# Performance work log

Hardware: AMD Instinct MI355X
Metric: run time of the kernel (lower is better)

The kernel has to match this reference:

```python
import jax, jax.numpy as jnp
import numpy as np

B = 16384      # games
BS = 19        # board size
N2 = BS * BS   # 361
G = 8          # groups per board
S = 4          # stones per group
R = B * G      # total groups
K = R * S      # total stones
M = N2         # hash history length (H*W*history_factor)
I32MIN = np.iinfo(np.int32).min
I32MAX = np.iinfo(np.int32).max
NEG = jnp.float32(-1e9)


def setup_inputs() -> dict:
    key = jax.random.key(0)
    ks = jax.random.split(key, 10)
    logits = jax.random.normal(ks[0], (B, BS, BS), dtype=jnp.float32)
    legal_mask = jax.random.uniform(ks[1], (B, BS, BS)) < 0.7
    current_player = jax.random.randint(ks[2], (B,), 0, 2, dtype=jnp.int32)
    current_hash = jax.random.randint(ks[3], (B,), 0, I32MAX, dtype=jnp.int32)
    hash_history = jax.random.randint(ks[4], (B, M), 0, I32MAX, dtype=jnp.int32)
    move_count = jax.random.randint(ks[5], (B,), 0, M, dtype=jnp.int32)
    ZposT = jax.random.randint(ks[6], (3, N2), 0, I32MAX, dtype=jnp.int32)
    stone_global_index = jax.random.randint(ks[7], (K,), 0, N2, dtype=jnp.int32)
    stone_global_pointer = jnp.arange(R + 1, dtype=jnp.int32) * S          # CSR: stones per group
    group_global_pointer_per_board = jnp.arange(B + 1, dtype=jnp.int32) * G  # CSR: groups per board
    cap_idx = jax.random.randint(ks[8], (B, N2, 4), 0, G, dtype=jnp.int32)
    cap_on = jax.random.uniform(ks[9], (B, N2, 4)) < 0.05
    captured_group_local_index = jnp.where(cap_on, cap_idx, jnp.int32(-1))
    return {
        "logits": logits,
        "legal_mask": legal_mask,
        "current_player": current_player,
        "current_hash": current_hash,
        "hash_history": hash_history,
        "move_count": move_count,
        "ZposT": ZposT,
        "stone_global_index": stone_global_index,
        "stone_global_pointer": stone_global_pointer,
        "group_global_pointer_per_board": group_global_pointer_per_board,
        "captured_group_local_index": captured_group_local_index,
    }


def reference(logits, legal_mask, current_player, current_hash, hash_history,
              move_count, ZposT, stone_global_index, stone_global_pointer,
              group_global_pointer_per_board, captured_group_local_index):
    Bn, H, W = legal_mask.shape
    Rn = stone_global_pointer.shape[0] - 1
    Kn = stone_global_index.shape[0]
    z_empty, z_black, z_white = ZposT[0], ZposT[1], ZposT[2]

    # Placement delta: empty -> current player's stone, for every candidate point. (B, N2)
    placement_delta = z_empty[None, :] ^ jnp.where(
        (current_player == 0)[:, None], z_black[None, :], z_white[None, :])

    # Map each group -> board, each stone -> group (CSR expansion).
    groups_per_board = group_global_pointer_per_board[1:] - group_global_pointer_per_board[:-1]
    group_board = jnp.repeat(jnp.arange(Bn, dtype=jnp.int32), groups_per_board,
                             total_repeat_length=Rn)
    stones_per_group = stone_global_pointer[1:] - stone_global_pointer[:-1]
    group_for_stone = jnp.repeat(jnp.arange(Rn, dtype=jnp.int32), stones_per_group,
                                 total_repeat_length=Kn)
    stone_board = group_board[group_for_stone]

    # Per-stone removal delta: opponent stone -> empty.
    opp_for_stone = (1 - current_player)[stone_board]           # (K,)
    si = stone_global_index.astype(jnp.int32)
    z_opp = ZposT[1 + opp_for_stone, si]
    per_stone_delta = z_opp ^ z_empty[si]                        # (K,) int32

    # Segmented XOR reduction over each group's stones via XOR prefix scan.
    prefix = jax.lax.associative_scan(jnp.bitwise_xor, per_stone_delta)
    start = stone_global_pointer[:-1]
    end = stone_global_pointer[1:]
    end_val = prefix[jnp.clip(end - 1, 0)]
    start_val = jnp.where(start > 0, prefix[jnp.clip(start - 1, 0)], jnp.int32(0))
    group_xor = end_val ^ start_val                              # (R,) per-group removal delta

    # Gather capture deltas for up to 4 captured neighbor groups per candidate move.
    offs = group_global_pointer_per_board[:-1][:, None, None]    # (B,1,1)
    flat_ids = jnp.clip(captured_group_local_index, 0) + offs    # (B,N2,4)
    cap_vals = jnp.where(captured_group_local_index >= 0, group_xor[flat_ids], jnp.int32(0))
    capture_delta = cap_vals[..., 0] ^ cap_vals[..., 1] ^ cap_vals[..., 2] ^ cap_vals[..., 3]

    candidate = current_hash[:, None] ^ placement_delta ^ capture_delta  # (B, N2)

    # Super-ko repeat detection against hash history (mask, sort, searchsorted).
    Mh = hash_history.shape[1]
    valid = jnp.arange(Mh, dtype=jnp.int32)[None, :] < jnp.minimum(move_count, Mh)[:, None]
    masked_hist = jnp.where(valid, hash_history, jnp.int32(I32MIN))
    sorted_hist = jnp.sort(masked_hist, axis=1)
    idx = jnp.clip(
        jax.vmap(lambda h, c: jnp.searchsorted(h, c, side='right'))(sorted_hist, candidate) - 1,
        0)
    found = jnp.take_along_axis(sorted_hist, idx, axis=1)
    repeat = (found == candidate).reshape(Bn, H, W)

    final_mask = legal_mask & ~repeat
    return jnp.where(final_mask, logits, NEG)
```

## Files before the change

kernel.cpp:

```cpp
#include <hip/hip_runtime.h>
#include <stdint.h>

#define N2 361
#define TBL 1024u
#define TBL_MASK 1023u
#define EMPTY 0x80000000u
#define NEGV -998244352.0f

__global__ __launch_bounds__(256) void k_groups(
    const int* __restrict__ current_player,
    const int* __restrict__ ZposT,
    const int* __restrict__ stone_global_index,
    const int* __restrict__ stone_global_pointer,
    unsigned*  __restrict__ gx_out,
    const void* __restrict__ legal_raw,
    unsigned*  __restrict__ fmt_out,
    int packed_bits, int Rn)
{
    const int r = blockIdx.x * 256 + threadIdx.x;

    if (blockIdx.x == 0 && threadIdx.x < 64) {
        const int lane = threadIdx.x;
        const unsigned* lwd = (const unsigned*)legal_raw;
        const unsigned dv0 = lwd[lane];
        const unsigned dv1 = (lane < 27) ? lwd[64 + lane] : 0u;
        auto classify = [](unsigned v) -> unsigned {
            unsigned f = 0;
            #pragma unroll
            for (int j = 0; j < 4; ++j) {
                const unsigned bv = (v >> (8 * j)) & 0xFFu;
                if (bv > 1u) f |= 1u;
                if (j != 0 && bv != 0u) f |= 2u;
            }
            const unsigned x = v & 0xFFFFu, y = v >> 16;
            if ((x && x != 0x3F80u) || (y && y != 0x3F80u)) f |= 4u;
            if (x == 0x3F80u) f |= 8u;
            return f;
        };
        unsigned fcl = classify(dv0);
        if (lane < 27) fcl |= classify(dv1);
        unsigned fa = 0;
        fa |= __ballot(fcl & 1u) ? 1u : 0u;
        fa |= __ballot(fcl & 2u) ? 2u : 0u;
        fa |= __ballot(fcl & 4u) ? 4u : 0u;
        fa |= __ballot(fcl & 8u) ? 8u : 0u;
        unsigned fmt;
        if (packed_bits) fmt = 4u;
        else if (!(fa & 1u)) fmt = (fa & 2u) ? 1u : 0u;
        else if (!(fa & 4u)) fmt = (fa & 8u) ? 2u : 0u;
        else fmt = 1u;
        if (lane == 0) fmt_out[0] = fmt;
    }

    if (r < Rn) {
        const int sp0 = stone_global_pointer[r];
        const int sp1 = stone_global_pointer[r + 1];
        const int b   = r >> 3;
        const int cp  = current_player[b];
        const int opprow = (2 - cp) * N2;
        unsigned x = 0u;
        for (int k = sp0; k < sp1; ++k) {
            const int si = stone_global_index[k];
            x ^= (unsigned)ZposT[opprow + si] ^ (unsigned)ZposT[si];
        }
        gx_out[r] = x;
    }
}

__device__ __forceinline__ unsigned sel8(uint4 a, uint4 b, unsigned i) {
    const unsigned r01 = (i & 1u) ? a.y : a.x;
    const unsigned r23 = (i & 1u) ? a.w : a.z;
    const unsigned r45 = (i & 1u) ? b.y : b.x;
    const unsigned r67 = (i & 1u) ? b.w : b.z;
    const unsigned r03 = (i & 2u) ? r23 : r01;
    const unsigned r47 = (i & 2u) ? r67 : r45;
    return (i & 4u) ? r47 : r03;
}

__global__ __launch_bounds__(384) void k_board(
    const float* __restrict__ logits,
    const void*  __restrict__ legal_raw,
    const int*   __restrict__ current_hash,
    const int*   __restrict__ current_player,
    const int*   __restrict__ hash_history,
    const int*   __restrict__ move_count,
    const int*   __restrict__ ZposT,
    const int4*  __restrict__ captured4,
    const unsigned* __restrict__ gx_ws,
    const unsigned* __restrict__ fmt_ws,
    float* __restrict__ out)
{
    __shared__ unsigned s_tbl[TBL];

    const int b = blockIdx.x;
    const int t = threadIdx.x;
    const size_t bbase = (size_t)b * N2;
    const bool act = t < N2;
    const int tc = act ? t : (N2 - 1);
    const size_t q = bbase + tc;

    int cnt = move_count[b];
    cnt = cnt < 0 ? 0 : (cnt > N2 ? N2 : cnt);
    const int      fmt  = (int)fmt_ws[0];
    const unsigned ch   = (unsigned)current_hash[b];
    const int      cp   = current_player[b];
    const uint4    ga   = *(const uint4*)(gx_ws + b * 8);
    const uint4    gb   = *(const uint4*)(gx_ws + b * 8 + 4);
    const int      prow = (1 + cp) * N2;

    const int   hv  = hash_history[q];
    const int4  cap = captured4[q];
    const float lgt = logits[q];
    unsigned    leg;
    if (fmt == 0)      leg = ((const unsigned*)legal_raw)[q];
    else if (fmt == 1) leg = ((const uint8_t*)legal_raw)[q];
    else if (fmt == 2) leg = ((const uint16_t*)legal_raw)[q];
    else               leg = (((const uint8_t*)legal_raw)[q >> 3] >> (q & 7)) & 1u;
    const unsigned zz = (unsigned)ZposT[tc] ^ (unsigned)ZposT[prow + tc];

    s_tbl[t] = EMPTY;
    s_tbl[t + 384] = EMPTY;
    if (t < (int)TBL - 768) s_tbl[t + 768] = EMPTY;
    __syncthreads();

    if (t < cnt) {
        const unsigned v = (unsigned)hv;
        unsigned slot = v & TBL_MASK;
        while (true) {
            const unsigned old = atomicCAS(&s_tbl[slot], EMPTY, v);
            if (old == EMPTY || old == v) break;
            slot = (slot + 1) & TBL_MASK;
        }
    }

    unsigned capd = 0u;
    if (cap.x >= 0) capd ^= sel8(ga, gb, (unsigned)cap.x & 7u);
    if (cap.y >= 0) capd ^= sel8(ga, gb, (unsigned)cap.y & 7u);
    if (cap.z >= 0) capd ^= sel8(ga, gb, (unsigned)cap.z & 7u);
    if (cap.w >= 0) capd ^= sel8(ga, gb, (unsigned)cap.w & 7u);
    const unsigned cand = ch ^ zz ^ capd;

    __syncthreads();

    bool rep = false;
    {
        unsigned slot = cand & TBL_MASK;
        while (true) {
            const unsigned v = s_tbl[slot];
            if (v == cand) { rep = true; break; }
            if (v == EMPTY) break;
            slot = (slot + 1) & TBL_MASK;
        }
    }

    if (act) {
        const float v = (leg && !rep) ? lgt : NEGV;
        __builtin_nontemporal_store(v, &out[q]);
    }
}

extern "C" void kernel_launch(void* const* d_in, const int* in_sizes, int n_in,
                              void* d_out, int out_size, void* d_ws, size_t ws_size,
                              hipStream_t stream) {
    const float* logits  = (const float*)d_in[0];
    const void*  legal   = (const void*)d_in[1];
    const int*   cur_pl  = (const int*)d_in[2];
    const int*   cur_h   = (const int*)d_in[3];
    const int*   hist    = (const int*)d_in[4];
    const int*   mcount  = (const int*)d_in[5];
    const int*   zpos    = (const int*)d_in[6];
    const int*   sgi     = (const int*)d_in[7];
    const int*   sgp     = (const int*)d_in[8];
    const int4*  cap4    = (const int4*)d_in[10];
    float*       out     = (float*)d_out;

    const int B  = in_sizes[2];
    const int Rn = in_sizes[8] - 1;
    const int packed = (in_sizes[1] != in_sizes[0]);

    unsigned* gx_ws  = (unsigned*)d_ws;
    unsigned* fmt_ws = (unsigned*)((char*)d_ws + (size_t)Rn * 4);

    k_groups<<<(Rn + 255) / 256, 256, 0, stream>>>(
        cur_pl, zpos, sgi, sgp, gx_ws, legal, fmt_ws, packed, Rn);

    k_board<<<B, 384, 0, stream>>>(
        logits, legal, cur_h, cur_pl, hist, mcount, zpos,
        cap4, gx_ws, fmt_ws, out);
}
```

Measured before the change: 218.3 us.

## Make board kernel persistent with double-buffered hash table and register prefetch

```diff
diff --git a/kernel.cpp b/kernel.cpp
--- a/kernel.cpp
+++ b/kernel.cpp
@@ -6,6 +6,7 @@
 #define TBL_MASK 1023u
 #define EMPTY 0x80000000u
 #define NEGV -998244352.0f
+#define NBLK 1280
 
 __global__ __launch_bounds__(256) void k_groups(
     const int* __restrict__ current_player,
@@ -77,6 +78,13 @@
     return (i & 4u) ? r47 : r03;
 }
 
+__device__ __forceinline__ unsigned load_leg(int fmt, const void* p, size_t q) {
+    if (fmt == 0)      return ((const unsigned*)p)[q];
+    else if (fmt == 1) return ((const uint8_t*)p)[q];
+    else if (fmt == 2) return ((const uint16_t*)p)[q];
+    else               return (((const uint8_t*)p)[q >> 3] >> (q & 7)) & 1u;
+}
+
 __global__ __launch_bounds__(384) void k_board(
     const float* __restrict__ logits,
     const void*  __restrict__ legal_raw,
@@ -88,74 +96,98 @@
     const int4*  __restrict__ captured4,
     const unsigned* __restrict__ gx_ws,
     const unsigned* __restrict__ fmt_ws,
-    float* __restrict__ out)
+    float* __restrict__ out,
+    int B, int nblk)
 {
-    __shared__ unsigned s_tbl[TBL];
-
-    const int b = blockIdx.x;
-    const int t = threadIdx.x;
-    const size_t bbase = (size_t)b * N2;
+    __shared__ unsigned s_tbl[2 * TBL];
+
+    const int t   = threadIdx.x;
     const bool act = t < N2;
-    const int tc = act ? t : (N2 - 1);
-    const size_t q = bbase + tc;
-
-    int cnt = move_count[b];
-    cnt = cnt < 0 ? 0 : (cnt > N2 ? N2 : cnt);
-    const int      fmt  = (int)fmt_ws[0];
-    const unsigned ch   = (unsigned)current_hash[b];
-    const int      cp   = current_player[b];
-    const uint4    ga   = *(const uint4*)(gx_ws + b * 8);
-    const uint4    gb   = *(const uint4*)(gx_ws + b * 8 + 4);
-    const int      prow = (1 + cp) * N2;
-
-    const int   hv  = hash_history[q];
-    const int4  cap = captured4[q];
-    const float lgt = logits[q];
-    unsigned    leg;
-    if (fmt == 0)      leg = ((const unsigned*)legal_raw)[q];
-    else if (fmt == 1) leg = ((const uint8_t*)legal_raw)[q];
-    else if (fmt == 2) leg = ((const uint16_t*)legal_raw)[q];
-    else               leg = (((const uint8_t*)legal_raw)[q >> 3] >> (q & 7)) & 1u;
-    const unsigned zz = (unsigned)ZposT[tc] ^ (unsigned)ZposT[prow + tc];
-
-    s_tbl[t] = EMPTY;
-    s_tbl[t + 384] = EMPTY;
-    if (t < (int)TBL - 768) s_tbl[t + 768] = EMPTY;
+    const int tc  = act ? t : (N2 - 1);
+    const int fmt = (int)fmt_ws[0];
+
+    for (int i = t; i < (int)(2 * TBL); i += 384) s_tbl[i] = EMPTY;
+
+    int b = blockIdx.x;
+    size_t q = (size_t)b * N2 + tc;
+    int      hv  = hash_history[q];
+    int4     cap = captured4[q];
+    float    lgt = logits[q];
+    unsigned leg = load_leg(fmt, legal_raw, q);
+    int      cnt = move_count[b];
+    unsigned ch  = (unsigned)current_hash[b];
+    int      cp  = current_player[b];
+    uint4    ga  = *(const uint4*)(gx_ws + (size_t)b * 8);
+    uint4    gb  = *(const uint4*)(gx_ws + (size_t)b * 8 + 4);
+
     __syncthreads();
 
-    if (t < cnt) {
-        const unsigned v = (unsigned)hv;
-        unsigned slot = v & TBL_MASK;
-        while (true) {
-            const unsigned old = atomicCAS(&s_tbl[slot], EMPTY, v);
-            if (old == EMPTY || old == v) break;
-            slot = (slot + 1) & TBL_MASK;
-        }
-    }
-
-    unsigned capd = 0u;
-    if (cap.x >= 0) capd ^= sel8(ga, gb, (unsigned)cap.x & 7u);
-    if (cap.y >= 0) capd ^= sel8(ga, gb, (unsigned)cap.y & 7u);
-    if (cap.z >= 0) capd ^= sel8(ga, gb, (unsigned)cap.z & 7u);
-    if (cap.w >= 0) capd ^= sel8(ga, gb, (unsigned)cap.w & 7u);
-    const unsigned cand = ch ^ zz ^ capd;
-
-    __syncthreads();
-
-    bool rep = false;
-    {
-        unsigned slot = cand & TBL_MASK;
-        while (true) {
-            const unsigned v = s_tbl[slot];
-            if (v == cand) { rep = true; break; }
-            if (v == EMPTY) break;
-            slot = (slot + 1) & TBL_MASK;
-        }
-    }
-
-    if (act) {
-        const float v = (leg && !rep) ? lgt : NEGV;
-        __builtin_nontemporal_store(v, &out[q]);
+    int it = 0;
+    while (true) {
+        unsigned* tbl = s_tbl + (unsigned)(it & 1) * TBL;
+        const int  nb   = b + nblk;
+        const bool more = nb < B;
+        const int  pb   = more ? nb : b;
+        const size_t pq = (size_t)pb * N2 + tc;
+
+        const int      nhv  = hash_history[pq];
+        const int4     ncap = captured4[pq];
+        const float    nlgt = logits[pq];
+        const unsigned nleg = load_leg(fmt, legal_raw, pq);
+        const int      ncnt = move_count[pb];
+        const unsigned nch  = (unsigned)current_hash[pb];
+        const int      ncp  = current_player[pb];
+        const uint4    nga  = *(const uint4*)(gx_ws + (size_t)pb * 8);
+        const uint4    ngb  = *(const uint4*)(gx_ws + (size_t)pb * 8 + 4);
+        asm volatile("" ::: "memory");
+
+        int ccnt = cnt < 0 ? 0 : (cnt > N2 ? N2 : cnt);
+        if (t < ccnt) {
+            const unsigned v = (unsigned)hv;
+            unsigned slot = v & TBL_MASK;
+            while (true) {
+                const unsigned old = atomicCAS(&tbl[slot], EMPTY, v);
+                if (old == EMPTY || old == v) break;
+                slot = (slot + 1) & TBL_MASK;
+            }
+        }
+
+        const int prow = (1 + cp) * N2;
+        const unsigned zz = (unsigned)ZposT[tc] ^ (unsigned)ZposT[prow + tc];
+        unsigned capd = 0u;
+        if (cap.x >= 0) capd ^= sel8(ga, gb, (unsigned)cap.x & 7u);
+        if (cap.y >= 0) capd ^= sel8(ga, gb, (unsigned)cap.y & 7u);
+        if (cap.z >= 0) capd ^= sel8(ga, gb, (unsigned)cap.z & 7u);
+        if (cap.w >= 0) capd ^= sel8(ga, gb, (unsigned)cap.w & 7u);
+        const unsigned cand = ch ^ zz ^ capd;
+
+        __syncthreads();
+
+        bool rep = false;
+        if (act) {
+            unsigned slot = cand & TBL_MASK;
+            while (true) {
+                const unsigned v = tbl[slot];
+                if (v == cand) { rep = true; break; }
+                if (v == EMPTY) break;
+                slot = (slot + 1) & TBL_MASK;
+            }
+            const float v = (leg && !rep) ? lgt : NEGV;
+            __builtin_nontemporal_store(v, &out[(size_t)b * N2 + tc]);
+        }
+
+        __syncthreads();
+
+        {
+            tbl[t] = EMPTY;
+            tbl[t + 384] = EMPTY;
+            if (t < (int)TBL - 768) tbl[t + 768] = EMPTY;
+        }
+
+        if (!more) break;
+        b = nb; hv = nhv; cap = ncap; lgt = nlgt; leg = nleg;
+        cnt = ncnt; ch = nch; cp = ncp; ga = nga; gb = ngb;
+        ++it;
     }
 }
 
@@ -184,7 +216,8 @@
     k_groups<<<(Rn + 255) / 256, 256, 0, stream>>>(
         cur_pl, zpos, sgi, sgp, gx_ws, legal, fmt_ws, packed, Rn);
 
-    k_board<<<B, 384, 0, stream>>>(
+    const int nblk = (B < NBLK) ? B : NBLK;
+    k_board<<<nblk, 384, 0, stream>>>(
         logits, legal, cur_h, cur_pl, hist, mcount, zpos,
-        cap4, gx_ws, fmt_ws, out);
-}
+        cap4, gx_ws, fmt_ws, out, B, nblk);
+}
```

Result: slower. 225.2 us (+3.2%).
